# Kernel tuning notes

Hardware: AMD Instinct MI355X
Metric: run time of the kernel (lower is better)

Reference implementation:

```python
import jax, jax.numpy as jnp
import numpy as np
from jax import lax

N, C, H, W = 16384, 1, 28, 28
HID = 128
EPS = 1e-5


def setup_inputs() -> dict:
    key = jax.random.key(0)
    ks = jax.random.split(key, 12)
    x = jax.random.normal(ks[0], (N, C, H, W), jnp.float32)
    w1 = jax.random.normal(ks[1], (8, 1, 7, 7), jnp.float32) * 0.05
    g1 = 1.0 + 0.1 * jax.random.normal(ks[2], (8,), jnp.float32)
    b1 = 0.1 * jax.random.normal(ks[3], (8,), jnp.float32)
    w2 = jax.random.normal(ks[4], (10, 8, 5, 5), jnp.float32) * 0.05
    g2 = 1.0 + 0.1 * jax.random.normal(ks[5], (10,), jnp.float32)
    b2 = 0.1 * jax.random.normal(ks[6], (10,), jnp.float32)
    w3 = jax.random.normal(ks[7], (HID, 10, 1, 1), jnp.float32) * 0.05
    g3 = 1.0 + 0.1 * jax.random.normal(ks[8], (HID,), jnp.float32)
    b3 = 0.1 * jax.random.normal(ks[9], (HID,), jnp.float32)
    # original inits fc weight to 0 and bias to identity affine; we add a small
    # random weight so theta varies per sample (exercises the sampler)
    fw = jax.random.normal(ks[10], (6, HID), jnp.float32) * 0.01
    fb = jnp.array([1, 0, 0, 0, 1, 0], jnp.float32)
    return {"x": x, "w1": w1, "g1": g1, "b1": b1, "w2": w2, "g2": g2,
            "b2": b2, "w3": w3, "g3": g3, "b3": b3, "fw": fw, "fb": fb}


def conv2d(x, w):
    return lax.conv_general_dilated(x, w, (1, 1), 'VALID',
                                    dimension_numbers=('NCHW', 'OIHW', 'NCHW'))


def batchnorm(x, g, b):
    m = jnp.mean(x, axis=(0, 2, 3), keepdims=True)
    v = jnp.mean((x - m) ** 2, axis=(0, 2, 3), keepdims=True)
    xh = (x - m) * lax.rsqrt(v + EPS)
    return xh * g[None, :, None, None] + b[None, :, None, None]


def maxpool2(x):
    return lax.reduce_window(x, -jnp.inf, lax.max, (1, 1, 2, 2), (1, 1, 2, 2), 'VALID')


def bilinear_sample(img_nhwc, grid):
    # img_nhwc: [N,H,W,C], grid: [N,H,W,2] normalized coords (x, y) in [-1,1]
    ix = (grid[..., 0] + 1.0) * 0.5 * (W - 1)
    iy = (grid[..., 1] + 1.0) * 0.5 * (H - 1)
    x0f = jnp.floor(ix); y0f = jnp.floor(iy)
    wx = ix - x0f; wy = iy - y0f
    x0 = jnp.clip(x0f.astype(jnp.int32), 0, W - 1)
    x1 = jnp.clip(x0 + 1, 0, W - 1)
    y0 = jnp.clip(y0f.astype(jnp.int32), 0, H - 1)
    y1 = jnp.clip(y0 + 1, 0, H - 1)

    def gather(img, yy, xx):  # img [H,W,C], yy/xx [H,W] -> [H,W,C]
        return img[yy, xx]
    g = jax.vmap(gather)
    v00 = g(img_nhwc, y0, x0)
    v01 = g(img_nhwc, y0, x1)
    v10 = g(img_nhwc, y1, x0)
    v11 = g(img_nhwc, y1, x1)
    wx = wx[..., None]; wy = wy[..., None]
    top = v00 * (1 - wx) + v01 * wx
    bot = v10 * (1 - wx) + v11 * wx
    return top * (1 - wy) + bot * wy


def reference(x, w1, g1, b1, w2, g2, b2, w3, g3, b3, fw, fb):
    # localization network
    xs = jax.nn.relu(maxpool2(batchnorm(conv2d(x, w1), g1, b1)))   # [N,8,11,11]
    xs = jax.nn.relu(maxpool2(batchnorm(conv2d(xs, w2), g2, b2)))  # [N,10,3,3]
    xs = jax.nn.relu(batchnorm(conv2d(xs, w3), g3, b3))            # [N,128,3,3]
    xs = jnp.mean(xs, axis=(2, 3))                                 # avgpool 3x3 -> [N,128]
    theta = (xs @ fw.T + fb).reshape(-1, 2, 3)                     # [N,2,3]
    # affine grid over normalized coords
    lin_x = jnp.linspace(-1.0, 1.0, W)
    lin_y = jnp.linspace(-1.0, 1.0, H)
    gx, gy = jnp.meshgrid(lin_x, lin_y)                            # [H,W]
    base = jnp.stack([gx, gy, jnp.ones_like(gx)], axis=-1)         # [H,W,3]
    grid = jnp.einsum('nij,hwj->nhwi', theta, base)                # [N,H,W,2]
    # sample in NHWC (matches the transpose dance in the torch code)
    out = bilinear_sample(jnp.transpose(x, (0, 2, 3, 1)), grid)
    return jnp.transpose(out, (0, 3, 1, 2))                        # back to NCHW
```

## Files before the change

kernel.cpp:

```cpp
#include <hip/hip_runtime.h>


static constexpr float kEPS = 1e-5f;

#define O_SUM1 0
#define O_SSQ1 8
#define O_SUM2 16
#define O_SSQ2 26
#define O_MOM  36
#define O_W2T  104
#define O_THETA 2112
#define O_E1   100864
#define O_E2   15960576
#define O_E2T  17435136

__global__ __launch_bounds__(256) void k_init(const float* __restrict__ w2,
                                              float* __restrict__ ws){
  int i = blockIdx.x*256 + threadIdx.x;
  if (i < 104) ws[i] = 0.f;
  if (i < 2000){
    int ic = i & 7;
    int r  = i >> 3;
    int kx = r % 5; r /= 5;
    int ky = r % 5; r /= 5;
    int oc = r;
    ws[O_W2T + i] = w2[(oc*8 + ic)*25 + ky*5 + kx];
  }
}

__global__ __launch_bounds__(256) void k_conv1(const float* __restrict__ x,
                                               const float* __restrict__ w1,
                                               const float* __restrict__ g1,
                                               float* __restrict__ ws){
  __shared__ float sw[392];
  const int tid = threadIdx.x;
  for (int i = tid; i < 392; i += 256) sw[i] = w1[i];
  __syncthreads();
  const int gid = blockIdx.x*256 + tid;
  const int c = gid & 7;
  const int r = gid >> 3;
  const int p = r % 11;
  const int n = r / 11;
  const float* __restrict__ xs = x + n*784;
  const float* __restrict__ wc = sw + c*49;
  const bool pos = (g1[c] >= 0.f);
  float* __restrict__ outp = ws + O_E1 + n*968 + p*88 + c;
  float sum=0.f, ssq=0.f;
  float a0[22], a1[22];
  #pragma unroll
  for (int i=0;i<22;i++){ a0[i]=0.f; a1[i]=0.f; }
  #pragma unroll
  for (int j=0;j<8;j++){
    float in[28];
    const float4* __restrict__ rp = (const float4*)(xs + (2*p+j)*28);
    #pragma unroll
    for (int q=0;q<7;q++){
      float4 v = rp[q];
      in[4*q]=v.x; in[4*q+1]=v.y; in[4*q+2]=v.z; in[4*q+3]=v.w;
    }
    if (j < 7){
      #pragma unroll
      for (int kx=0;kx<7;kx++){
        float wv = wc[j*7+kx];
        #pragma unroll
        for (int xo=0;xo<22;xo++) a0[xo] = fmaf(wv, in[xo+kx], a0[xo]);
      }
    }
    if (j >= 1){
      #pragma unroll
      for (int kx=0;kx<7;kx++){
        float wv = wc[(j-1)*7+kx];
        #pragma unroll
        for (int xo=0;xo<22;xo++) a1[xo] = fmaf(wv, in[xo+kx], a1[xo]);
      }
    }
  }
  #pragma unroll
  for (int xo=0;xo<22;xo++){
    sum += a0[xo] + a1[xo];
    ssq = fmaf(a0[xo],a0[xo],ssq);
    ssq = fmaf(a1[xo],a1[xo],ssq);
  }
  #pragma unroll
  for (int px=0;px<11;px++){
    float m4 = fmaxf(fmaxf(a0[2*px],a0[2*px+1]), fmaxf(a1[2*px],a1[2*px+1]));
    float n4 = fminf(fminf(a0[2*px],a0[2*px+1]), fminf(a1[2*px],a1[2*px+1]));
    outp[px*8] = pos ? m4 : n4;
  }
  sum += __shfl_xor(sum,8);  ssq += __shfl_xor(ssq,8);
  sum += __shfl_xor(sum,16); ssq += __shfl_xor(ssq,16);
  sum += __shfl_xor(sum,32); ssq += __shfl_xor(ssq,32);
  __shared__ float ls[16];
  if (tid < 16) ls[tid] = 0.f;
  __syncthreads();
  if ((tid & 63) < 8){
    atomicAdd(&ls[tid & 7], sum);
    atomicAdd(&ls[8 + (tid & 7)], ssq);
  }
  __syncthreads();
  if (tid < 16) atomicAdd(&ws[O_SUM1 + tid], ls[tid]);
}

__global__ __launch_bounds__(256) void k_conv2(float* __restrict__ ws,
                                               const float* __restrict__ g1,
                                               const float* __restrict__ b1,
                                               const float* __restrict__ g2){
  __shared__ float sw2[2160];
  for (int i = threadIdx.x; i < 2000; i += 256){
    int oc_ = i/200, r = i - oc_*200;
    sw2[oc_*216 + r] = ws[O_W2T + i];
  }
  __syncthreads();
  float s1r[8], t1r[8];
  {
    const float invM1 = 1.f/7929856.f;
    #pragma unroll
    for (int c=0;c<8;c++){
      float mean = ws[O_SUM1+c]*invM1;
      float var  = ws[O_SSQ1+c]*invM1 - mean*mean;
      float sc = g1[c]*rsqrtf(var + kEPS);
      s1r[c] = sc; t1r[c] = b1[c] - mean*sc;
    }
  }
  const int blk = blockIdx.x;
  const int half = (blk >= 640) ? 1 : 0;
  const int gid = (blk - half*640)*256 + threadIdx.x;
  const int n = gid/10, oc = gid - 10*n;
  const int r0 = half*4;
  const int nrows = half ? 7 : 8;
  const float* __restrict__ wt = sw2 + oc*216;
  const float* __restrict__ base = ws + O_E1 + n*968;
  float acc[28];
  #pragma unroll
  for (int i=0;i<28;i++) acc[i]=0.f;
  for (int jj=0; jj<nrows; ++jj){
    const int iy = r0 + jj;
    #pragma unroll
    for (int icl=0; icl<2; ++icl){
      float4 in4[11];
      #pragma unroll
      for (int q=0;q<11;q++){
        float4 v = *(const float4*)(base + iy*88 + q*8 + icl*4);
        in4[q].x = fmaxf(fmaf(s1r[icl*4+0], v.x, t1r[icl*4+0]), 0.f);
        in4[q].y = fmaxf(fmaf(s1r[icl*4+1], v.y, t1r[icl*4+1]), 0.f);
        in4[q].z = fmaxf(fmaf(s1r[icl*4+2], v.z, t1r[icl*4+2]), 0.f);
        in4[q].w = fmaxf(fmaf(s1r[icl*4+3], v.w, t1r[icl*4+3]), 0.f);
      }
      #pragma unroll
      for (int ol=0; ol<4; ++ol){
        if (half && ol==3) continue;
        const int ky = jj - ol;
        if (ky < 0 || ky > 4) continue;
        const float* __restrict__ wrow = wt + ky*40 + icl*4;
        #pragma unroll
        for (int kx=0;kx<5;kx++){
          float4 w = *(const float4*)(wrow + kx*8);
          #pragma unroll
          for (int ox=0;ox<7;ox++){
            float a = acc[ol*7+ox];
            a = fmaf(w.x, in4[ox+kx].x, a);
            a = fmaf(w.y, in4[ox+kx].y, a);
            a = fmaf(w.z, in4[ox+kx].z, a);
            a = fmaf(w.w, in4[ox+kx].w, a);
            acc[ol*7+ox] = a;
          }
        }
      }
    }
  }
  {
    const int NV = (half ? 3 : 4)*7;
    float sum=0.f, ssq=0.f;
    #pragma unroll
    for (int i=0;i<28;i++){
      if (i < NV){ float v = acc[i]; sum += v; ssq = fmaf(v,v,ssq); }
    }
    __shared__ float ls[20];
    if (threadIdx.x < 20) ls[threadIdx.x] = 0.f;
    __syncthreads();
    atomicAdd(&ls[oc], sum);
    atomicAdd(&ls[10+oc], ssq);
    __syncthreads();
    if (threadIdx.x < 20) atomicAdd(&ws[O_SUM2 + threadIdx.x], ls[threadIdx.x]);
  }
  {
    const bool pos = (g2[oc] >= 0.f);
    const int npy = half ? 1 : 2;
    #pragma unroll
    for (int pl=0; pl<2; pl++){
      if (pl >= npy) continue;
      const int py = half ? 2 : pl;
      #pragma unroll
      for (int px=0;px<3;px++){
        float v00 = acc[(2*pl)*7   + 2*px], v01 = acc[(2*pl)*7   + 2*px+1];
        float v10 = acc[(2*pl+1)*7 + 2*px], v11 = acc[(2*pl+1)*7 + 2*px+1];
        float m4 = fmaxf(fmaxf(v00,v01), fmaxf(v10,v11));
        float n4 = fminf(fminf(v00,v01), fminf(v10,v11));
        ws[O_E2 + (n*9 + py*3 + px)*10 + oc] = pos ? m4 : n4;
      }
    }
  }
}

__global__ __launch_bounds__(256) void k_pool2fin(float* __restrict__ ws,
                                                  const float* __restrict__ g2,
                                                  const float* __restrict__ b2){
  __shared__ float smom[65];
  const int tid = threadIdx.x;
  if (tid < 65) smom[tid] = 0.f;
  __syncthreads();
  const float invM = 1.f/802816.f;
  const int gid = blockIdx.x*256 + tid;
  const int n = gid/9, p = gid - n*9;
  const float* __restrict__ src = ws + O_E2 + gid*10;
  float xv[10];
  #pragma unroll
  for (int c=0;c<10;c++){
    float mean = ws[O_SUM2+c]*invM;
    float var  = ws[O_SSQ2+c]*invM - mean*mean;
    float sc = g2[c]*rsqrtf(var + kEPS);
    float tc = b2[c] - mean*sc;
    float v = fmaxf(fmaf(sc, src[c], tc), 0.f);
    xv[c] = v;
    ws[O_E2T + (p*10 + c)*16384 + n] = v;
  }
  float mu[10], sm[55];
  #pragma unroll
  for (int i=0;i<10;i++) mu[i] = xv[i];
  #pragma unroll
  for (int i=0;i<10;i++){
    #pragma unroll
    for (int j=i;j<10;j++) sm[i*10 - i*(i-1)/2 + (j-i)] = xv[i]*xv[j];
  }
  #pragma unroll
  for (int off=1; off<64; off<<=1){
    #pragma unroll
    for (int i=0;i<10;i++) mu[i] += __shfl_xor(mu[i], off);
    #pragma unroll
    for (int k=0;k<55;k++) sm[k] += __shfl_xor(sm[k], off);
  }
  if ((tid & 63) == 0){
    #pragma unroll
    for (int i=0;i<10;i++) atomicAdd(&smom[i], mu[i]);
    #pragma unroll
    for (int k=0;k<55;k++) atomicAdd(&smom[10+k], sm[k]);
  }
  __syncthreads();
  if (tid < 65) atomicAdd(&ws[O_MOM + tid], smom[tid]);
}

__global__ __launch_bounds__(64) void k_theta(float* __restrict__ ws,
                                              const float* __restrict__ w3,
                                              const float* __restrict__ g3,
                                              const float* __restrict__ b3,
                                              const float* __restrict__ fw,
                                              const float* __restrict__ fb){
  __shared__ float s3[128], t3[128];
  const int tid = threadIdx.x;
  #pragma unroll
  for (int rep=0; rep<2; rep++){
    const int oc = tid + rep*64;
    const float invM = 1.f/147456.f;
    float mu[10], w[10];
    #pragma unroll
    for (int i=0;i<10;i++) mu[i] = ws[O_MOM+i]*invM;
    #pragma unroll
    for (int i=0;i<10;i++) w[i] = w3[oc*10+i];
    float mean3 = 0.f;
    #pragma unroll
    for (int i=0;i<10;i++) mean3 += w[i]*mu[i];
    float var3 = 0.f;
    #pragma unroll
    for (int i=0;i<10;i++){
      #pragma unroll
      for (int j=i;j<10;j++){
        float Sij = ws[O_MOM+10 + i*10 - i*(i-1)/2 + (j-i)]*invM;
        float cov = Sij - mu[i]*mu[j];
        float coef = (i==j) ? 1.f : 2.f;
        var3 += coef * w[i] * w[j] * cov;
      }
    }
    var3 = fmaxf(var3, 0.f);
    float s = g3[oc]*rsqrtf(var3 + kEPS);
    s3[oc] = s;
    t3[oc] = b3[oc] - mean3*s;
  }
  __syncthreads();
  const int n = blockIdx.x*64 + tid;
  float in[90];
  #pragma unroll
  for (int i=0;i<90;i++) in[i] = ws[O_E2T + i*16384 + n];
  float th[6];
  #pragma unroll
  for (int j=0;j<6;j++) th[j] = fb[j];
  for (int oc=0; oc<128; oc++){
    float s = s3[oc], t = t3[oc];
    float fsum = 0.f;
    #pragma unroll
    for (int p=0;p<9;p++){
      float v = 0.f;
      #pragma unroll
      for (int ic=0;ic<10;ic++) v = fmaf(w3[oc*10+ic], in[p*10+ic], v);
      fsum += fmaxf(fmaf(s,v,t), 0.f);
    }
    float feat = fsum * (1.f/9.f);
    #pragma unroll
    for (int j=0;j<6;j++) th[j] = fmaf(fw[j*128+oc], feat, th[j]);
  }
  float* __restrict__ op = ws + O_THETA + n*6;
  #pragma unroll
  for (int j=0;j<6;j++) op[j] = th[j];
}

__global__ __launch_bounds__(256) void k_sample(const float* __restrict__ x,
                                                const float* __restrict__ ws,
                                                float* __restrict__ out){
  const int n = blockIdx.x;
  __shared__ float sx[784];
  const int tid = threadIdx.x;
  if (tid < 196) ((float4*)sx)[tid] = ((const float4*)(x + n*784))[tid];
  __syncthreads();
  const float* __restrict__ th = ws + O_THETA + n*6;
  const float t0=th[0], t1=th[1], t2=th[2], t3=th[3], t4=th[4], t5=th[5];
  float* __restrict__ op = out + n*784;
  for (int idx=tid; idx<784; idx+=256){
    int h = idx/28;
    int wcol = idx - 28*h;
    float gx = fmaf((float)wcol, 2.f/27.f, -1.f);
    float gy = fmaf((float)h,    2.f/27.f, -1.f);
    float ix = (fmaf(t0,gx,fmaf(t1,gy,t2)) + 1.f)*13.5f;
    float iy = (fmaf(t3,gx,fmaf(t4,gy,t5)) + 1.f)*13.5f;
    float x0f = floorf(ix), y0f = floorf(iy);
    float wx = ix - x0f, wy = iy - y0f;
    int x0 = min(max((int)x0f,0),27); int x1 = min(x0+1,27);
    int y0 = min(max((int)y0f,0),27); int y1 = min(y0+1,27);
    float v00 = sx[y0*28+x0], v01 = sx[y0*28+x1];
    float v10 = sx[y1*28+x0], v11 = sx[y1*28+x1];
    float top = v00*(1.f-wx) + v01*wx;
    float bot = v10*(1.f-wx) + v11*wx;
    op[idx] = top*(1.f-wy) + bot*wy;
  }
}

extern "C" void kernel_launch(void* const* d_in, const int* in_sizes, int n_in,
                              void* d_out, int out_size, void* d_ws, size_t ws_size,
                              hipStream_t stream){
  (void)in_sizes; (void)n_in; (void)out_size; (void)ws_size;
  const float* x  = (const float*)d_in[0];
  const float* w1 = (const float*)d_in[1];
  const float* g1 = (const float*)d_in[2];
  const float* b1 = (const float*)d_in[3];
  const float* w2 = (const float*)d_in[4];
  const float* g2 = (const float*)d_in[5];
  const float* b2 = (const float*)d_in[6];
  const float* w3 = (const float*)d_in[7];
  const float* g3 = (const float*)d_in[8];
  const float* b3 = (const float*)d_in[9];
  const float* fw = (const float*)d_in[10];
  const float* fb = (const float*)d_in[11];
  float* ws  = (float*)d_ws;
  float* out = (float*)d_out;

  hipLaunchKernelGGL(k_init,      dim3(8),     dim3(256), 0, stream, w2, ws);
  hipLaunchKernelGGL(k_conv1,     dim3(5632),  dim3(256), 0, stream, x, w1, g1, ws);
  hipLaunchKernelGGL(k_conv2,     dim3(1280),  dim3(256), 0, stream, ws, g1, b1, g2);
  hipLaunchKernelGGL(k_pool2fin,  dim3(576),   dim3(256), 0, stream, ws, g2, b2);
  hipLaunchKernelGGL(k_theta,     dim3(256),   dim3(64),  0, stream, ws, w3, g3, b3, fw, fb);
  hipLaunchKernelGGL(k_sample,    dim3(16384), dim3(256), 0, stream, x, ws, out);
}
```

Before: 376.5 us.

## Restructure conv2 to compute one output row for all channels per thread

Conv2 now assigns each thread one (sample, output row) pair and computes all 10 output channels, so each input row loaded from conv1 is reused across channels instead of being reloaded by 10 threads. Weights are read straight from global memory through uniform addresses rather than staged in LDS. The full 7x7x10 pre-pool conv2 output is written to a larger workspace buffer, and the max/min pooling moves into k_pool2fin. BN statistics are reduced with a wave-level shuffle and one atomic per wave. In exchange, the thread holds 70 accumulators, which raises register pressure, and more intermediate data goes to memory.

Measured after the change: 734.5 us. +95.1%, slower.

```diff
diff --git a/kernel.cpp b/kernel.cpp
--- a/kernel.cpp
+++ b/kernel.cpp
@@ -11,8 +11,8 @@
 #define O_W2T  104
 #define O_THETA 2112
 #define O_E1   100864
-#define O_E2   15960576
-#define O_E2T  17435136
+#define O_C2   15960576
+#define O_E2T  23988736
 
 __global__ __launch_bounds__(256) void k_init(const float* __restrict__ w2,
                                               float* __restrict__ ws){
@@ -101,16 +101,9 @@
   if (tid < 16) atomicAdd(&ws[O_SUM1 + tid], ls[tid]);
 }
 
-__global__ __launch_bounds__(256) void k_conv2(float* __restrict__ ws,
-                                               const float* __restrict__ g1,
-                                               const float* __restrict__ b1,
-                                               const float* __restrict__ g2){
-  __shared__ float sw2[2160];
-  for (int i = threadIdx.x; i < 2000; i += 256){
-    int oc_ = i/200, r = i - oc_*200;
-    sw2[oc_*216 + r] = ws[O_W2T + i];
-  }
-  __syncthreads();
+__global__ __launch_bounds__(64) void k_conv2(float* __restrict__ ws,
+                                              const float* __restrict__ g1,
+                                              const float* __restrict__ b1){
   float s1r[8], t1r[8];
   {
     const float invM1 = 1.f/7929856.f;
@@ -122,82 +115,70 @@
       s1r[c] = sc; t1r[c] = b1[c] - mean*sc;
     }
   }
-  const int blk = blockIdx.x;
-  const int half = (blk >= 640) ? 1 : 0;
-  const int gid = (blk - half*640)*256 + threadIdx.x;
-  const int n = gid/10, oc = gid - 10*n;
-  const int r0 = half*4;
-  const int nrows = half ? 7 : 8;
-  const float* __restrict__ wt = sw2 + oc*216;
-  const float* __restrict__ base = ws + O_E1 + n*968;
-  float acc[28];
-  #pragma unroll
-  for (int i=0;i<28;i++) acc[i]=0.f;
-  for (int jj=0; jj<nrows; ++jj){
-    const int iy = r0 + jj;
-    #pragma unroll
-    for (int icl=0; icl<2; ++icl){
+  const int gid = blockIdx.x*64 + threadIdx.x;
+  const int n = gid/7, r = gid - n*7;
+  const float* __restrict__ w2t = ws + O_W2T;
+  const float* __restrict__ base = ws + O_E1 + n*968 + r*88;
+  float acc[70];
+  #pragma unroll
+  for (int i=0;i<70;i++) acc[i]=0.f;
+  for (int ky=0; ky<5; ky++){
+    for (int ich=0; ich<2; ich++){
       float4 in4[11];
       #pragma unroll
       for (int q=0;q<11;q++){
-        float4 v = *(const float4*)(base + iy*88 + q*8 + icl*4);
-        in4[q].x = fmaxf(fmaf(s1r[icl*4+0], v.x, t1r[icl*4+0]), 0.f);
-        in4[q].y = fmaxf(fmaf(s1r[icl*4+1], v.y, t1r[icl*4+1]), 0.f);
-        in4[q].z = fmaxf(fmaf(s1r[icl*4+2], v.z, t1r[icl*4+2]), 0.f);
-        in4[q].w = fmaxf(fmaf(s1r[icl*4+3], v.w, t1r[icl*4+3]), 0.f);
-      }
-      #pragma unroll
-      for (int ol=0; ol<4; ++ol){
-        if (half && ol==3) continue;
-        const int ky = jj - ol;
-        if (ky < 0 || ky > 4) continue;
-        const float* __restrict__ wrow = wt + ky*40 + icl*4;
+        float4 v = *(const float4*)(base + ky*88 + q*8 + ich*4);
+        in4[q].x = fmaxf(fmaf(s1r[ich*4+0], v.x, t1r[ich*4+0]), 0.f);
+        in4[q].y = fmaxf(fmaf(s1r[ich*4+1], v.y, t1r[ich*4+1]), 0.f);
+        in4[q].z = fmaxf(fmaf(s1r[ich*4+2], v.z, t1r[ich*4+2]), 0.f);
+        in4[q].w = fmaxf(fmaf(s1r[ich*4+3], v.w, t1r[ich*4+3]), 0.f);
+      }
+      const float* __restrict__ wb = w2t + ky*40 + ich*4;
+      #pragma unroll
+      for (int oc=0;oc<10;oc++){
         #pragma unroll
         for (int kx=0;kx<5;kx++){
-          float4 w = *(const float4*)(wrow + kx*8);
+          float4 w = *(const float4*)(wb + oc*200 + kx*8);
           #pragma unroll
-          for (int ox=0;ox<7;ox++){
-            float a = acc[ol*7+ox];
-            a = fmaf(w.x, in4[ox+kx].x, a);
-            a = fmaf(w.y, in4[ox+kx].y, a);
-            a = fmaf(w.z, in4[ox+kx].z, a);
-            a = fmaf(w.w, in4[ox+kx].w, a);
-            acc[ol*7+ox] = a;
+          for (int xx=0;xx<7;xx++){
+            float a = acc[oc*7+xx];
+            a = fmaf(w.x, in4[xx+kx].x, a);
+            a = fmaf(w.y, in4[xx+kx].y, a);
+            a = fmaf(w.z, in4[xx+kx].z, a);
+            a = fmaf(w.w, in4[xx+kx].w, a);
+            acc[oc*7+xx] = a;
           }
         }
       }
     }
   }
-  {
-    const int NV = (half ? 3 : 4)*7;
-    float sum=0.f, ssq=0.f;
-    #pragma unroll
-    for (int i=0;i<28;i++){
-      if (i < NV){ float v = acc[i]; sum += v; ssq = fmaf(v,v,ssq); }
-    }
-    __shared__ float ls[20];
-    if (threadIdx.x < 20) ls[threadIdx.x] = 0.f;
-    __syncthreads();
-    atomicAdd(&ls[oc], sum);
-    atomicAdd(&ls[10+oc], ssq);
-    __syncthreads();
-    if (threadIdx.x < 20) atomicAdd(&ws[O_SUM2 + threadIdx.x], ls[threadIdx.x]);
-  }
-  {
-    const bool pos = (g2[oc] >= 0.f);
-    const int npy = half ? 1 : 2;
-    #pragma unroll
-    for (int pl=0; pl<2; pl++){
-      if (pl >= npy) continue;
-      const int py = half ? 2 : pl;
-      #pragma unroll
-      for (int px=0;px<3;px++){
-        float v00 = acc[(2*pl)*7   + 2*px], v01 = acc[(2*pl)*7   + 2*px+1];
-        float v10 = acc[(2*pl+1)*7 + 2*px], v11 = acc[(2*pl+1)*7 + 2*px+1];
-        float m4 = fmaxf(fmaxf(v00,v01), fmaxf(v10,v11));
-        float n4 = fminf(fminf(v00,v01), fminf(v10,v11));
-        ws[O_E2 + (n*9 + py*3 + px)*10 + oc] = pos ? m4 : n4;
-      }
+  float* __restrict__ op = ws + O_C2 + n*490 + r*70;
+  #pragma unroll
+  for (int xx=0;xx<7;xx++){
+    #pragma unroll
+    for (int oc=0;oc<10;oc++) op[xx*10+oc] = acc[oc*7+xx];
+  }
+  float sum[10], ssq[10];
+  #pragma unroll
+  for (int oc=0;oc<10;oc++){
+    float s=0.f, q=0.f;
+    #pragma unroll
+    for (int xx=0;xx<7;xx++){ float v=acc[oc*7+xx]; s+=v; q=fmaf(v,v,q); }
+    sum[oc]=s; ssq[oc]=q;
+  }
+  #pragma unroll
+  for (int off=1; off<64; off<<=1){
+    #pragma unroll
+    for (int oc=0;oc<10;oc++){
+      sum[oc] += __shfl_xor(sum[oc], off);
+      ssq[oc] += __shfl_xor(ssq[oc], off);
+    }
+  }
+  if (threadIdx.x == 0){
+    #pragma unroll
+    for (int oc=0;oc<10;oc++){
+      atomicAdd(&ws[O_SUM2+oc], sum[oc]);
+      atomicAdd(&ws[O_SSQ2+oc], ssq[oc]);
     }
   }
 }
@@ -212,7 +193,8 @@
   const float invM = 1.f/802816.f;
   const int gid = blockIdx.x*256 + tid;
   const int n = gid/9, p = gid - n*9;
-  const float* __restrict__ src = ws + O_E2 + gid*10;
+  const int py = p/3, px = p - 3*py;
+  const float* __restrict__ src = ws + O_C2 + n*490 + py*140 + px*20;
   float xv[10];
   #pragma unroll
   for (int c=0;c<10;c++){
@@ -220,7 +202,11 @@
     float var  = ws[O_SSQ2+c]*invM - mean*mean;
     float sc = g2[c]*rsqrtf(var + kEPS);
     float tc = b2[c] - mean*sc;
-    float v = fmaxf(fmaf(sc, src[c], tc), 0.f);
+    float v00 = src[c], v01 = src[10+c], v10 = src[70+c], v11 = src[80+c];
+    float m4 = fmaxf(fmaxf(v00,v01), fmaxf(v10,v11));
+    float n4 = fminf(fminf(v00,v01), fminf(v10,v11));
+    float ext = (sc >= 0.f) ? m4 : n4;
+    float v = fmaxf(fmaf(sc, ext, tc), 0.f);
     xv[c] = v;
     ws[O_E2T + (p*10 + c)*16384 + n] = v;
   }
@@ -363,7 +349,7 @@
 
   hipLaunchKernelGGL(k_init,      dim3(8),     dim3(256), 0, stream, w2, ws);
   hipLaunchKernelGGL(k_conv1,     dim3(5632),  dim3(256), 0, stream, x, w1, g1, ws);
-  hipLaunchKernelGGL(k_conv2,     dim3(1280),  dim3(256), 0, stream, ws, g1, b1, g2);
+  hipLaunchKernelGGL(k_conv2,     dim3(1792),  dim3(64),  0, stream, ws, g1, b1);
   hipLaunchKernelGGL(k_pool2fin,  dim3(576),   dim3(256), 0, stream, ws, g2, b2);
   hipLaunchKernelGGL(k_theta,     dim3(256),   dim3(64),  0, stream, ws, w3, g3, b3, fw, fb);
   hipLaunchKernelGGL(k_sample,    dim3(16384), dim3(256), 0, stream, x, ws, out);
```
